# Kernel optimization log

Measured on AMD Instinct MI355X. Metric: run time of the kernel, lower is better.

Reference implementation:

```python
import jax, jax.numpy as jnp
import numpy as np

BETA = 0.2

def setup_inputs() -> dict:
    key = jax.random.key(0)
    k1, k2 = jax.random.split(key)
    z = jax.random.normal(k1, (32, 256, 32, 32), dtype=jnp.float32)
    # codebook initialized uniform(-1/K, 1/K) as in the torch module
    K, D = 8192, 256
    codebook = jax.random.uniform(k2, (K, D), dtype=jnp.float32, minval=-1.0 / K, maxval=1.0 / K)
    return {"z": z, "codebook": codebook}

def reference(z, codebook):
    b, d, h, w = z.shape
    # (b d h w) -> (b*h*w, d)
    zf = jnp.transpose(z, (0, 2, 3, 1)).reshape(-1, d)
    # squared L2 distances to codebook entries: [N, K]
    dist = (
        jnp.sum(zf * zf, axis=1, keepdims=True)
        + jnp.sum(codebook * codebook, axis=1)
        - 2.0 * jnp.matmul(zf, codebook.T)
    )
    indices = jnp.argmin(dist, axis=1)  # [N]
    # gather == one-hot matmul in value (and in gradient wrt codebook)
    quantized = jnp.take(codebook, indices, axis=0)  # [N, d]
    codebook_loss = jnp.mean((jax.lax.stop_gradient(zf) - quantized) ** 2)
    commitment_loss = BETA * jnp.mean((zf - jax.lax.stop_gradient(quantized)) ** 2)
    # straight-through estimator
    q_st = zf + jax.lax.stop_gradient(quantized - zf)
    q_st = jnp.transpose(q_st.reshape(b, h, w, d), (0, 3, 1, 2))
    return (q_st, codebook_loss, commitment_loss)
```

## Files before the change

### kernel.cpp

```cpp
#include <hip/hip_runtime.h>
#include <hip/hip_bf16.h>
#include <stdint.h>

typedef __attribute__((ext_vector_type(4))) float floatx4;
typedef __attribute__((ext_vector_type(16))) float floatx16;
typedef __attribute__((ext_vector_type(4))) int intx4;
typedef __attribute__((ext_vector_type(8))) int intx8;
typedef __attribute__((ext_vector_type(2))) unsigned int uint2v;
typedef unsigned long long u64;

typedef __attribute__((address_space(1))) const uint32_t ga_u32;
typedef __attribute__((address_space(3))) uint32_t ls_u32;

static constexpr int NROWS = 32768;
static constexpr int NCODE = 8192;
static constexpr int QELEMS = 8388608;
static constexpr float CSCALE = 8192.0f;

__global__ __launch_bounds__(256) void prep_all(
    const float* __restrict__ z, const float* __restrict__ cb,
    unsigned char* __restrict__ z8, unsigned char* __restrict__ c8,
    float* __restrict__ norms, u64* __restrict__ amin)
{
  const int bid = blockIdx.x;
  const int t = threadIdx.x;
  if (bid < 1024) {
    __shared__ float tile[32][260];
    const int b = bid & 31, db = (bid >> 5) & 7, hwb = bid >> 8;
    const int d0 = db * 32, hw0 = hwb * 256;
    const float* src = z + (((size_t)b * 256 + d0) << 10) + hw0;
#pragma unroll
    for (int i = 0; i < 8; ++i) {
      int idx = i * 256 + t;
      int r = idx >> 6, c4 = (idx & 63) * 4;
      *(floatx4*)&tile[r][c4] = *(const floatx4*)&src[((size_t)r << 10) + c4];
    }
    __syncthreads();
    const int dq = t & 3;
    const int hb = t >> 2;
#pragma unroll
    for (int it = 0; it < 4; ++it) {
      int h = hb + it * 64;
      float f[8];
#pragma unroll
      for (int i = 0; i < 8; ++i) f[i] = tile[dq * 8 + i][h];
      int lo = __builtin_amdgcn_cvt_pk_fp8_f32(f[0], f[1], 0, false);
      lo = __builtin_amdgcn_cvt_pk_fp8_f32(f[2], f[3], lo, true);
      int hi = __builtin_amdgcn_cvt_pk_fp8_f32(f[4], f[5], 0, false);
      hi = __builtin_amdgcn_cvt_pk_fp8_f32(f[6], f[7], hi, true);
      uint2v o; o[0] = (unsigned)lo; o[1] = (unsigned)hi;
      *(uint2v*)&z8[((size_t)(b * 1024 + hw0 + h)) * 256 + d0 + dq * 8] = o;
    }
  } else if (bid < 3072) {
    const int k = (bid - 1024) * 4 + (t >> 6);
    const int lane = t & 63;
    floatx4 v = *(const floatx4*)&cb[((size_t)k << 8) + lane * 4];
    float a = v[0] * CSCALE, b2 = v[1] * CSCALE, c = v[2] * CSCALE, d2 = v[3] * CSCALE;
    int r = __builtin_amdgcn_cvt_pk_fp8_f32(a, b2, 0, false);
    r = __builtin_amdgcn_cvt_pk_fp8_f32(c, d2, r, true);
    *(unsigned int*)&c8[((size_t)k << 8) + lane * 4] = (unsigned)r;
    float s = a * a + b2 * b2 + c * c + d2 * d2;
#pragma unroll
    for (int off = 32; off; off >>= 1) s += __shfl_down(s, off);
    if (lane == 0) norms[k] = s;
  } else {
    const int base = (bid - 3072) * 2048;
#pragma unroll
    for (int i = 0; i < 8; ++i) amin[base + i * 256 + t] = ~0ull;
  }
}

__global__ __launch_bounds__(256, 2) void gemm_argmin(
    const unsigned char* __restrict__ z8, const unsigned char* __restrict__ c8,
    const float* __restrict__ norms, u64* __restrict__ amin)
{
  __shared__ alignas(16) unsigned char lds8[3 * 24576 + 4096];

  const int tid = threadIdx.x;
  const int lane = tid & 63;
  const int wid = tid >> 6;
  const int wm = wid >> 1;
  const int wn = wid & 1;

  const int bid = blockIdx.x;
  const int swz = (bid & 7) * 1024 + (bid >> 3);
  const int cx = swz & 63;
  const int cy = swz >> 6;
  const int m0 = cx * 128;
  const int n0 = cy * 256;

  const int l31 = lane & 31;
  const int hi = lane >> 5;
  const int k2 = hi << 1;

  floatx16 acc[2][4];
#pragma unroll
  for (int i = 0; i < 2; ++i)
#pragma unroll
    for (int j = 0; j < 4; ++j)
#pragma unroll
      for (int e = 0; e < 16; ++e) acc[i][j][e] = 0.f;

  auto STAGE = [&](int kt) {
    unsigned char* sbase = lds8 + (kt % 3) * 24576;
#pragma unroll
    for (int p = 0; p < 2; ++p) {
      int flat = p * 256 + tid;
      int row = flat >> 2, s = flat & 3;
      int ps = s ^ ((row >> 1) & 3);
      const unsigned char* gp = c8 + ((size_t)(m0 + row) << 8) + kt * 64 + ps * 16;
      __builtin_amdgcn_global_load_lds((ga_u32*)gp, (ls_u32*)(sbase + flat * 16), 16, 0, 0);
    }
#pragma unroll
    for (int p = 0; p < 4; ++p) {
      int flat = p * 256 + tid;
      int row = flat >> 2, s = flat & 3;
      int ps = s ^ ((row >> 1) & 3);
      const unsigned char* gp = z8 + ((size_t)(n0 + row) << 8) + kt * 64 + ps * 16;
      __builtin_amdgcn_global_load_lds((ga_u32*)gp, (ls_u32*)(sbase + 8192 + flat * 16), 16, 0, 0);
    }
  };

  auto RDOP = [&](const unsigned char* rbase, int row) -> intx8 {
    const int v = (row >> 1) & 3;
    intx4 lo = *(const intx4*)(rbase + row * 64 + ((k2 ^ v) << 4));
    intx4 hv = *(const intx4*)(rbase + row * 64 + (((k2 + 1) ^ v) << 4));
    intx8 o;
#pragma unroll
    for (int w = 0; w < 4; ++w) { o[w] = lo[w]; o[4 + w] = hv[w]; }
    return o;
  };

  STAGE(0); STAGE(1);
  asm volatile("s_waitcnt vmcnt(6)" ::: "memory");
  __builtin_amdgcn_s_barrier();
  asm volatile("" ::: "memory");

#pragma unroll
  for (int kt = 0; kt < 4; ++kt) {
    unsigned char* sbase = lds8 + (kt % 3) * 24576;
    intx8 af[2], bf[4];
#pragma unroll
    for (int ti = 0; ti < 2; ++ti)
      af[ti] = RDOP(sbase, wm * 64 + ti * 32 + l31);
#pragma unroll
    for (int tj = 0; tj < 4; ++tj)
      bf[tj] = RDOP(sbase + 8192, wn * 128 + tj * 32 + l31);
    if (kt < 2) STAGE(kt + 2);
    __builtin_amdgcn_s_setprio(1);
#pragma unroll
    for (int ti = 0; ti < 2; ++ti)
#pragma unroll
      for (int tj = 0; tj < 4; ++tj)
        acc[ti][tj] = __builtin_amdgcn_mfma_scale_f32_32x32x64_f8f6f4(
            af[ti], bf[tj], acc[ti][tj], 0, 0, 0, 127, 0, 127);
    __builtin_amdgcn_s_setprio(0);
    if (kt < 2)       asm volatile("s_waitcnt vmcnt(6)" ::: "memory");
    else if (kt == 2) asm volatile("s_waitcnt vmcnt(0)" ::: "memory");
    if (kt < 3) {
      asm volatile("" ::: "memory");
      __builtin_amdgcn_s_barrier();
      asm volatile("" ::: "memory");
    }
  }

  floatx4 nv[2][4];
#pragma unroll
  for (int ti = 0; ti < 2; ++ti)
#pragma unroll
    for (int rq = 0; rq < 4; ++rq)
      nv[ti][rq] = *(const floatx4*)&norms[m0 + wm * 64 + ti * 32 + rq * 8 + 4 * hi];

  u64* best2 = (u64*)(lds8 + 3 * 24576);
#pragma unroll
  for (int tj = 0; tj < 4; ++tj) {
    float best = __builtin_inff();
    int bc = 0;
#pragma unroll
    for (int ti = 0; ti < 2; ++ti)
#pragma unroll
      for (int rq = 0; rq < 4; ++rq)
#pragma unroll
        for (int rl = 0; rl < 4; ++rl) {
          float sc = fmaf(acc[ti][tj][rq * 4 + rl], -16384.f, nv[ti][rq][rl]);
          int cd = m0 + wm * 64 + ti * 32 + rq * 8 + 4 * hi + rl;
          if (sc < best) { best = sc; bc = cd; }
        }
    uint32_t u = __float_as_uint(best);
    u ^= ((uint32_t)((int32_t)u >> 31) | 0x80000000u);
    u64 p = ((u64)u << 32) | (uint32_t)bc;
    {
      u64 o = (u64)__shfl_xor((long long)p, 32);
      p = o < p ? o : p;
    }
    if (lane < 32) best2[(size_t)(wn * 128 + tj * 32 + l31) * 2 + wm] = p;
  }
  __syncthreads();
  {
    u64 a = best2[tid * 2], b = best2[tid * 2 + 1];
    u64 p = a < b ? a : b;
    atomicMin(&amin[n0 + tid], p);
  }
}

__global__ __launch_bounds__(256) void gather_out(
    const float* __restrict__ z, const float* __restrict__ cb,
    const u64* __restrict__ amin,
    float* __restrict__ out, float* __restrict__ partial)
{
  const int t = threadIdx.x;
  const size_t e0 = ((size_t)blockIdx.x * 256 + t) * 8;
  const int d = (int)((e0 >> 10) & 255);
  const int b = (int)(e0 >> 18);
  const int n0 = b * 1024 + (int)(e0 & 1023);
  uint32_t kv[8];
#pragma unroll
  for (int m = 0; m < 8; ++m) kv[m] = (uint32_t)amin[n0 + m];
  floatx4 z0 = *(const floatx4*)&z[e0];
  floatx4 z1 = *(const floatx4*)&z[e0 + 4];
  floatx4 q0, q1;
#pragma unroll
  for (int m = 0; m < 4; ++m) {
    q0[m] = cb[((size_t)kv[m] << 8) + d];
    q1[m] = cb[((size_t)kv[4 + m] << 8) + d];
  }
  *(floatx4*)&out[e0] = q0;
  *(floatx4*)&out[e0 + 4] = q1;
  float s = 0.f;
#pragma unroll
  for (int m = 0; m < 4; ++m) {
    float d0 = z0[m] - q0[m], d1 = z1[m] - q1[m];
    s += d0 * d0 + d1 * d1;
  }
#pragma unroll
  for (int off = 32; off; off >>= 1) s += __shfl_down(s, off);
  __shared__ float ps[4];
  if ((t & 63) == 0) ps[t >> 6] = s;
  __syncthreads();
  if (t == 0) partial[blockIdx.x] = ps[0] + ps[1] + ps[2] + ps[3];
}

__global__ __launch_bounds__(256) void finalize(const float* __restrict__ partial,
                                                float* __restrict__ out)
{
  const int t = threadIdx.x;
  float s = 0.f;
#pragma unroll
  for (int i = 0; i < 16; ++i) s += partial[i * 256 + t];
#pragma unroll
  for (int off = 32; off; off >>= 1) s += __shfl_down(s, off);
  __shared__ float ps[4];
  if ((t & 63) == 0) ps[t >> 6] = s;
  __syncthreads();
  if (t == 0) {
    float m = (ps[0] + ps[1] + ps[2] + ps[3]) / (float)QELEMS;
    out[QELEMS] = m;
    out[QELEMS + 1] = 0.2f * m;
  }
}

extern "C" void kernel_launch(void* const* d_in, const int* in_sizes, int n_in,
                              void* d_out, int out_size, void* d_ws, size_t ws_size,
                              hipStream_t stream)
{
  const float* z = (const float*)d_in[0];
  const float* cb = (const float*)d_in[1];
  float* out = (float*)d_out;
  char* ws = (char*)d_ws;

  unsigned char* z8 = (unsigned char*)(ws + 0);
  unsigned char* c8 = (unsigned char*)(ws + 8388608);
  float* norms = (float*)(ws + 10485760);
  u64* amin = (u64*)(ws + 10616832);
  float* lpart = (float*)(ws + 10878976);

  prep_all<<<3088, 256, 0, stream>>>(z, cb, z8, c8, norms, amin);
  gemm_argmin<<<8192, 256, 0, stream>>>(z8, c8, norms, amin);
  gather_out<<<QELEMS / 2048, 256, 0, stream>>>(z, cb, amin, out, lpart);
  finalize<<<1, 256, 0, stream>>>(lpart, out);
}
```

Before: 161.0 us.

## Load codebook operands directly to registers and stage full z tile in LDS

Replaces the three-stage K-pipelined LDS staging with a single bulk load. Each wave reads its codebook A fragments for all four K steps straight from global memory into registers. The whole 256x256 z8 tile is copied to LDS at once with a wider XOR swizzle, leaving one barrier instead of several per K step. This gives up load/compute overlap and the setprio hints in exchange for less LDS traffic and synchronisation, and raises register pressure and LDS use (~68KB), which may hurt occupancy at two blocks per CU.

```diff
diff --git a/kernel.cpp b/kernel.cpp
--- a/kernel.cpp
+++ b/kernel.cpp
@@ -74,7 +74,7 @@
     const unsigned char* __restrict__ z8, const unsigned char* __restrict__ c8,
     const float* __restrict__ norms, u64* __restrict__ amin)
 {
-  __shared__ alignas(16) unsigned char lds8[3 * 24576 + 4096];
+  __shared__ alignas(16) unsigned char lds8[65536 + 4096];
 
   const int tid = threadIdx.x;
   const int lane = tid & 63;
@@ -93,85 +93,73 @@
   const int hi = lane >> 5;
   const int k2 = hi << 1;
 
-  floatx16 acc[2][4];
-#pragma unroll
-  for (int i = 0; i < 2; ++i)
-#pragma unroll
-    for (int j = 0; j < 4; ++j)
-#pragma unroll
-      for (int e = 0; e < 16; ++e) acc[i][j][e] = 0.f;
-
-  auto STAGE = [&](int kt) {
-    unsigned char* sbase = lds8 + (kt % 3) * 24576;
-#pragma unroll
-    for (int p = 0; p < 2; ++p) {
-      int flat = p * 256 + tid;
-      int row = flat >> 2, s = flat & 3;
-      int ps = s ^ ((row >> 1) & 3);
-      const unsigned char* gp = c8 + ((size_t)(m0 + row) << 8) + kt * 64 + ps * 16;
-      __builtin_amdgcn_global_load_lds((ga_u32*)gp, (ls_u32*)(sbase + flat * 16), 16, 0, 0);
-    }
-#pragma unroll
-    for (int p = 0; p < 4; ++p) {
-      int flat = p * 256 + tid;
-      int row = flat >> 2, s = flat & 3;
-      int ps = s ^ ((row >> 1) & 3);
-      const unsigned char* gp = z8 + ((size_t)(n0 + row) << 8) + kt * 64 + ps * 16;
-      __builtin_amdgcn_global_load_lds((ga_u32*)gp, (ls_u32*)(sbase + 8192 + flat * 16), 16, 0, 0);
-    }
-  };
-
-  auto RDOP = [&](const unsigned char* rbase, int row) -> intx8 {
-    const int v = (row >> 1) & 3;
-    intx4 lo = *(const intx4*)(rbase + row * 64 + ((k2 ^ v) << 4));
-    intx4 hv = *(const intx4*)(rbase + row * 64 + (((k2 + 1) ^ v) << 4));
-    intx8 o;
-#pragma unroll
-    for (int w = 0; w < 4; ++w) { o[w] = lo[w]; o[4 + w] = hv[w]; }
-    return o;
-  };
-
-  STAGE(0); STAGE(1);
-  asm volatile("s_waitcnt vmcnt(6)" ::: "memory");
+  intx8 af[2][4];
+#pragma unroll
+  for (int ti = 0; ti < 2; ++ti) {
+    const unsigned char* arow = c8 + ((size_t)(m0 + wm * 64 + ti * 32 + l31) << 8);
+#pragma unroll
+    for (int kt = 0; kt < 4; ++kt) {
+      intx4 lo = *(const intx4*)(arow + kt * 64 + k2 * 16);
+      intx4 hv = *(const intx4*)(arow + kt * 64 + k2 * 16 + 16);
+      intx8 o;
+#pragma unroll
+      for (int w = 0; w < 4; ++w) { o[w] = lo[w]; o[4 + w] = hv[w]; }
+      af[ti][kt] = o;
+    }
+  }
+
+  floatx4 nv[2][4];
+#pragma unroll
+  for (int ti = 0; ti < 2; ++ti)
+#pragma unroll
+    for (int rq = 0; rq < 4; ++rq)
+      nv[ti][rq] = *(const floatx4*)&norms[m0 + wm * 64 + ti * 32 + rq * 8 + 4 * hi];
+
+#pragma unroll
+  for (int p = 0; p < 16; ++p) {
+    int f = p * 256 + tid;
+    int row = f >> 4, sp = f & 15;
+    int ls = sp ^ ((row >> 1) & 7);
+    const unsigned char* gp = z8 + ((size_t)(n0 + row) << 8) + ls * 16;
+    __builtin_amdgcn_global_load_lds((ga_u32*)gp, (ls_u32*)(lds8 + f * 16), 16, 0, 0);
+  }
+  asm volatile("s_waitcnt vmcnt(0)" ::: "memory");
   __builtin_amdgcn_s_barrier();
   asm volatile("" ::: "memory");
 
+  floatx16 acc[2][4];
+#pragma unroll
+  for (int i = 0; i < 2; ++i)
+#pragma unroll
+    for (int j = 0; j < 4; ++j)
+#pragma unroll
+      for (int e = 0; e < 16; ++e) acc[i][j][e] = 0.f;
+
 #pragma unroll
   for (int kt = 0; kt < 4; ++kt) {
-    unsigned char* sbase = lds8 + (kt % 3) * 24576;
-    intx8 af[2], bf[4];
-#pragma unroll
-    for (int ti = 0; ti < 2; ++ti)
-      af[ti] = RDOP(sbase, wm * 64 + ti * 32 + l31);
-#pragma unroll
-    for (int tj = 0; tj < 4; ++tj)
-      bf[tj] = RDOP(sbase + 8192, wn * 128 + tj * 32 + l31);
-    if (kt < 2) STAGE(kt + 2);
-    __builtin_amdgcn_s_setprio(1);
+    intx8 bf[4];
+#pragma unroll
+    for (int tj = 0; tj < 4; ++tj) {
+      int row = wn * 128 + tj * 32 + l31;
+      const unsigned char* rbase = lds8 + row * 256;
+      int msk = (row >> 1) & 7;
+      int L0 = kt * 4 + k2;
+      intx4 lo = *(const intx4*)(rbase + ((L0 ^ msk) << 4));
+      intx4 hv = *(const intx4*)(rbase + (((L0 + 1) ^ msk) << 4));
+      intx8 o;
+#pragma unroll
+      for (int w = 0; w < 4; ++w) { o[w] = lo[w]; o[4 + w] = hv[w]; }
+      bf[tj] = o;
+    }
 #pragma unroll
     for (int ti = 0; ti < 2; ++ti)
 #pragma unroll
       for (int tj = 0; tj < 4; ++tj)
         acc[ti][tj] = __builtin_amdgcn_mfma_scale_f32_32x32x64_f8f6f4(
-            af[ti], bf[tj], acc[ti][tj], 0, 0, 0, 127, 0, 127);
-    __builtin_amdgcn_s_setprio(0);
-    if (kt < 2)       asm volatile("s_waitcnt vmcnt(6)" ::: "memory");
-    else if (kt == 2) asm volatile("s_waitcnt vmcnt(0)" ::: "memory");
-    if (kt < 3) {
-      asm volatile("" ::: "memory");
-      __builtin_amdgcn_s_barrier();
-      asm volatile("" ::: "memory");
-    }
-  }
-
-  floatx4 nv[2][4];
-#pragma unroll
-  for (int ti = 0; ti < 2; ++ti)
-#pragma unroll
-    for (int rq = 0; rq < 4; ++rq)
-      nv[ti][rq] = *(const floatx4*)&norms[m0 + wm * 64 + ti * 32 + rq * 8 + 4 * hi];
-
-  u64* best2 = (u64*)(lds8 + 3 * 24576);
+            af[ti][kt], bf[tj], acc[ti][tj], 0, 0, 0, 127, 0, 127);
+  }
+
+  u64* best2 = (u64*)(lds8 + 65536);
 #pragma unroll
   for (int tj = 0; tj < 4; ++tj) {
     float best = __builtin_inff();
```

Result: slower. 173.3 us (+7.7%).
